# Kernel optimization log

Measured on AMD Instinct MI355X. Metric: run time of the kernel, lower is better.

The kernel has to match this reference:

```python
import jax, jax.numpy as jnp
import numpy as np

HOPS = 3  # C[i].weight tied to A[i+1].weight -> HOPS+1 distinct tables E_0..E_HOPS


def setup_inputs() -> dict:
    key = jax.random.key(0)
    ks = jax.random.split(key, 10)
    B, M, K, E, G, V = 32, 2048, 4, 128, 128, 50000
    s = 1.0 / np.sqrt(E).astype(np.float32)
    context = jax.random.randint(ks[0], (B, M, K), 0, V)          # memory (triples)
    h_ = jax.random.normal(ks[1], (B, G), dtype=jnp.float32)      # prev GRU hidden
    y_ = jax.random.randint(ks[2], (B,), 0, V)                    # prev token
    emb = jax.random.normal(ks[3], (HOPS + 1, V, E), dtype=jnp.float32) * 0.1
    W_ih = jax.random.normal(ks[4], (3 * G, E), dtype=jnp.float32) * s
    W_hh = jax.random.normal(ks[5], (3 * G, G), dtype=jnp.float32) * s
    b_ih = jax.random.normal(ks[6], (3 * G,), dtype=jnp.float32) * s
    b_hh = jax.random.normal(ks[7], (3 * G,), dtype=jnp.float32) * s
    W_vocab = jax.random.normal(ks[8], (V, 2 * E), dtype=jnp.float32) * s
    b_vocab = jax.random.normal(ks[9], (V,), dtype=jnp.float32) * s
    return dict(context=context, h_=h_, y_=y_, emb=emb, W_ih=W_ih, W_hh=W_hh,
                b_ih=b_ih, b_hh=b_hh, W_vocab=W_vocab, b_vocab=b_vocab)


def gru_cell(x, h, W_ih, W_hh, b_ih, b_hh):
    # PyTorch GRU cell semantics (r, z, n gate order).
    gi = x @ W_ih.T + b_ih
    gh = h @ W_hh.T + b_hh
    i_r, i_z, i_n = jnp.split(gi, 3, axis=-1)
    h_r, h_z, h_n = jnp.split(gh, 3, axis=-1)
    r = jax.nn.sigmoid(i_r + h_r)
    z = jax.nn.sigmoid(i_z + h_z)
    n = jnp.tanh(i_n + r * h_n)
    return (1.0 - z) * n + z * h


def reference(context, h_, y_, emb, W_ih, W_hh, b_ih, b_hh, W_vocab, b_vocab):
    x = emb[0][y_]                                   # [B, E] A[0] embed of prev token
    h = gru_cell(x, h_, W_ih, W_hh, b_ih, b_hh)      # [B, G], G == E
    q = h
    o1 = None
    attn = None
    for hop in range(HOPS):
        mA = emb[hop][context].sum(axis=2)           # gather [B,M,K,E] -> sum over K -> [B,M,E]
        p = jnp.einsum('bme,be->bm', mA, q)          # attention scores over memory slots
        attn = jax.nn.softmax(p, axis=1)             # [B, M]
        mC = emb[hop + 1][context].sum(axis=2)       # C[hop] table (tied to A[hop+1])
        o = jnp.einsum('bm,bme->be', attn, mC)       # memory read [B, E]
        q = q + o
        if hop == 0:
            o1 = o
    logits = jnp.concatenate([h, o1], axis=1) @ W_vocab.T + b_vocab  # [B, V]
    p_vocab = jax.nn.softmax(logits, axis=1)
    return h, p_vocab, attn
```

## Files before the change

kernel.cpp:

```cpp
#include <hip/hip_runtime.h>
#include <math.h>

#define BB 32
#define MM 2048
#define KK 4
#define EE 128
#define GG 128
#define VV 50000
#define HOPS 3

__global__ __launch_bounds__(384) void gru_kernel(
    const float* __restrict__ emb0,
    const int*   __restrict__ y,
    const float* __restrict__ hprev,
    const float* __restrict__ W_ih,
    const float* __restrict__ W_hh,
    const float* __restrict__ b_ih,
    const float* __restrict__ b_hh,
    float* __restrict__ h_out,
    float* __restrict__ q,
    float* __restrict__ o1)
{
    int b = blockIdx.x;
    int t = threadIdx.x;
    __shared__ float x[EE], h[GG], gi[3*GG], gh[3*GG];
    if (t < EE)            x[t]       = emb0[(size_t)y[b]*EE + t];
    else if (t < 2*EE)     h[t-EE]    = hprev[b*GG + (t-EE)];
    if (t < EE) o1[b*EE + t] = 0.f;
    __syncthreads();
    {
        float accI = b_ih[t], accH = b_hh[t];
        const float* wi = W_ih + (size_t)t*EE;
        const float* wh = W_hh + (size_t)t*GG;
        #pragma unroll 8
        for (int e = 0; e < EE; e++) { accI += x[e]*wi[e]; accH += h[e]*wh[e]; }
        gi[t] = accI; gh[t] = accH;
    }
    __syncthreads();
    if (t < GG) {
        float r = 1.f/(1.f + __expf(-(gi[t]        + gh[t])));
        float z = 1.f/(1.f + __expf(-(gi[GG+t]     + gh[GG+t])));
        float n = tanhf(gi[2*GG+t] + r*gh[2*GG+t]);
        float hn = (1.f - z)*n + z*h[t];
        h_out[b*GG + t] = hn;
        q[b*GG + t]     = hn;
    }
}

__global__ __launch_bounds__(256) void scores_kernel(
    const float* __restrict__ embT,
    const int*   __restrict__ ctx,
    const float* __restrict__ q,
    float* __restrict__ p)
{
    int gid  = blockIdx.x * 4 + (threadIdx.x >> 6);
    int lane = threadIdx.x & 63;
    int b    = gid >> 11;
    const int4 c = *(const int4*)(ctx + (size_t)gid*KK);
    float2 qv = *(const float2*)(q + b*EE + lane*2);
    float2 v0 = *(const float2*)(embT + (size_t)c.x*EE + lane*2);
    float2 v1 = *(const float2*)(embT + (size_t)c.y*EE + lane*2);
    float2 v2 = *(const float2*)(embT + (size_t)c.z*EE + lane*2);
    float2 v3 = *(const float2*)(embT + (size_t)c.w*EE + lane*2);
    float sx = v0.x + v1.x + v2.x + v3.x;
    float sy = v0.y + v1.y + v2.y + v3.y;
    float acc = sx*qv.x + sy*qv.y;
    #pragma unroll
    for (int off = 32; off; off >>= 1) acc += __shfl_down(acc, off);
    if (lane == 0) p[gid] = acc;
}

__global__ __launch_bounds__(256) void scores_s_kernel(
    const float* __restrict__ S,
    const float* __restrict__ q,
    float* __restrict__ p)
{
    int gid  = blockIdx.x * 4 + (threadIdx.x >> 6);
    int lane = threadIdx.x & 63;
    int b    = gid >> 11;
    float2 sv = *(const float2*)(S + (size_t)gid*EE + lane*2);
    float2 qv = *(const float2*)(q + b*EE + lane*2);
    float acc = sv.x*qv.x + sv.y*qv.y;
    #pragma unroll
    for (int off = 32; off; off >>= 1) acc += __shfl_down(acc, off);
    if (lane == 0) p[gid] = acc;
}

template<int WRITE_S, int SAVE_O1>
__global__ __launch_bounds__(256) void oacc_fused_kernel(
    const float* __restrict__ embT,
    const int*   __restrict__ ctx,
    const float* __restrict__ p,
    float* __restrict__ S_out,
    float* __restrict__ q,
    float* __restrict__ o1)
{
    int blk = blockIdx.x;
    int b = blk >> 5, s = blk & 31;
    int t = threadIdx.x;
    int w = t >> 6, lane = t & 63;

    const float* row = p + (size_t)b*MM;
    float v[8];
    float mx = -INFINITY;
    #pragma unroll
    for (int i = 0; i < 8; i++) { v[i] = row[t + i*256]; mx = fmaxf(mx, v[i]); }
    __shared__ float red[6];
    #pragma unroll
    for (int off = 32; off; off >>= 1) mx = fmaxf(mx, __shfl_down(mx, off));
    if (lane == 0) red[w] = mx;
    __syncthreads();
    if (t == 0) red[4] = fmaxf(fmaxf(red[0],red[1]), fmaxf(red[2],red[3]));
    __syncthreads();
    mx = red[4];
    float sum = 0.f;
    #pragma unroll
    for (int i = 0; i < 8; i++) sum += __expf(v[i] - mx);
    #pragma unroll
    for (int off = 32; off; off >>= 1) sum += __shfl_down(sum, off);
    __syncthreads();
    if (lane == 0) red[w] = sum;
    __syncthreads();
    if (t == 0) red[5] = 1.f / (red[0]+red[1]+red[2]+red[3]);
    __syncthreads();
    float rs = red[5];

    int m0 = s*64 + w*16;
    float ax = 0.f, ay = 0.f;
    for (int i = 0; i < 16; i++) {
        int m = m0 + i;
        float a = __expf(row[m] - mx) * rs;
        const int4 c = *(const int4*)(ctx + (size_t)(b*MM + m)*KK);
        float2 v0 = *(const float2*)(embT + (size_t)c.x*EE + lane*2);
        float2 v1 = *(const float2*)(embT + (size_t)c.y*EE + lane*2);
        float2 v2 = *(const float2*)(embT + (size_t)c.z*EE + lane*2);
        float2 v3 = *(const float2*)(embT + (size_t)c.w*EE + lane*2);
        float sx = v0.x + v1.x + v2.x + v3.x;
        float sy = v0.y + v1.y + v2.y + v3.y;
        if (WRITE_S)
            *(float2*)(S_out + ((size_t)b*MM + m)*EE + lane*2) = make_float2(sx, sy);
        ax += a * sx;
        ay += a * sy;
    }
    __shared__ float acc_red[4][EE];
    acc_red[w][lane*2]   = ax;
    acc_red[w][lane*2+1] = ay;
    __syncthreads();
    if (t < EE) {
        float vv = acc_red[0][t] + acc_red[1][t] + acc_red[2][t] + acc_red[3][t];
        atomicAdd(&q[b*EE + t], vv);
        if (SAVE_O1) atomicAdd(&o1[b*EE + t], vv);
    }
}

__global__ __launch_bounds__(256) void softmax_m_kernel(
    const float* __restrict__ p,
    float* __restrict__ attn)
{
    int b = blockIdx.x, t = threadIdx.x;
    const float* row = p + (size_t)b*MM;
    float v[8];
    float mx = -INFINITY;
    #pragma unroll
    for (int i = 0; i < 8; i++) { v[i] = row[t + i*256]; mx = fmaxf(mx, v[i]); }
    __shared__ float red[6];
    int w = t >> 6, lane = t & 63;
    #pragma unroll
    for (int off = 32; off; off >>= 1) mx = fmaxf(mx, __shfl_down(mx, off));
    if (lane == 0) red[w] = mx;
    __syncthreads();
    if (t == 0) { float m2 = fmaxf(fmaxf(red[0],red[1]), fmaxf(red[2],red[3])); red[4] = m2; }
    __syncthreads();
    mx = red[4];
    float sum = 0.f;
    #pragma unroll
    for (int i = 0; i < 8; i++) { v[i] = __expf(v[i] - mx); sum += v[i]; }
    #pragma unroll
    for (int off = 32; off; off >>= 1) sum += __shfl_down(sum, off);
    if (lane == 0) red[w] = sum;
    __syncthreads();
    if (t == 0) { red[5] = 1.f / (red[0]+red[1]+red[2]+red[3]); }
    __syncthreads();
    float rs = red[5];
    #pragma unroll
    for (int i = 0; i < 8; i++) attn[(size_t)b*MM + t + i*256] = v[i]*rs;
}

__global__ __launch_bounds__(256) void logits_kernel(
    const float* __restrict__ h,
    const float* __restrict__ o1,
    const float* __restrict__ Wv,
    const float* __restrict__ bv,
    float* __restrict__ logits)
{
    __shared__ float Ut[256][32];
    __shared__ float Wt[32][132];
    int t = threadIdx.x;
    for (int i = t; i < 256*32; i += 256) {
        int e = i >> 5, b = i & 31;
        Ut[e][b] = (e < GG) ? h[b*GG + e] : o1[b*EE + (e - GG)];
    }
    int vg = t & 31;
    int bg = t >> 5;
    int v0 = blockIdx.x * 128;
    float acc[4][4];
    #pragma unroll
    for (int i = 0; i < 4; i++)
        #pragma unroll
        for (int j = 0; j < 4; j++) acc[i][j] = 0.f;

    int vrow = t >> 1;
    int half = t & 1;
    const float* wrow = Wv + (size_t)(v0 + vrow)*256 + half*16;
    bool vok = (v0 + vrow) < VV;

    for (int ec = 0; ec < 256; ec += 32) {
        __syncthreads();
        #pragma unroll
        for (int j = 0; j < 4; j++) {
            float4 w = make_float4(0.f, 0.f, 0.f, 0.f);
            if (vok) w = *(const float4*)(wrow + ec + j*4);
            int e0 = half*16 + j*4;
            Wt[e0+0][vrow] = w.x;
            Wt[e0+1][vrow] = w.y;
            Wt[e0+2][vrow] = w.z;
            Wt[e0+3][vrow] = w.w;
        }
        __syncthreads();
        #pragma unroll 8
        for (int e = 0; e < 32; e++) {
            float4 w = *(const float4*)(&Wt[e][vg*4]);
            float4 u = *(const float4*)(&Ut[ec + e][bg*4]);
            acc[0][0] += w.x*u.x; acc[0][1] += w.x*u.y; acc[0][2] += w.x*u.z; acc[0][3] += w.x*u.w;
            acc[1][0] += w.y*u.x; acc[1][1] += w.y*u.y; acc[1][2] += w.y*u.z; acc[1][3] += w.y*u.w;
            acc[2][0] += w.z*u.x; acc[2][1] += w.z*u.y; acc[2][2] += w.z*u.z; acc[2][3] += w.z*u.w;
            acc[3][0] += w.w*u.x; acc[3][1] += w.w*u.y; acc[3][2] += w.w*u.z; acc[3][3] += w.w*u.w;
        }
    }
    #pragma unroll
    for (int i = 0; i < 4; i++) {
        int v = v0 + vg*4 + i;
        if (v < VV) {
            float bb = bv[v];
            #pragma unroll
            for (int j = 0; j < 4; j++)
                logits[(size_t)(bg*4 + j)*VV + v] = acc[i][j] + bb;
        }
    }
}

#define VCHUNK 6250
__global__ __launch_bounds__(256) void vpart_kernel(
    const float* __restrict__ logits,
    float* __restrict__ part)
{
    int blk = blockIdx.x;
    int b = blk >> 3, c = blk & 7;
    int t = threadIdx.x;
    const float* row = logits + (size_t)b*VV;
    int start = c*VCHUNK;
    int end   = min(start + VCHUNK, VV);
    __shared__ float red[4];
    int w = t >> 6, lane = t & 63;
    float mx = -INFINITY;
    for (int i = start + t; i < end; i += 256) mx = fmaxf(mx, row[i]);
    #pragma unroll
    for (int off = 32; off; off >>= 1) mx = fmaxf(mx, __shfl_down(mx, off));
    if (lane == 0) red[w] = mx;
    __syncthreads();
    float m = fmaxf(fmaxf(red[0], red[1]), fmaxf(red[2], red[3]));
    float sum = 0.f;
    for (int i = start + t; i < end; i += 256) sum += __expf(row[i] - m);
    #pragma unroll
    for (int off = 32; off; off >>= 1) sum += __shfl_down(sum, off);
    __syncthreads();
    if (lane == 0) red[w] = sum;
    __syncthreads();
    if (t == 0) {
        part[blk*2]   = m;
        part[blk*2+1] = red[0] + red[1] + red[2] + red[3];
    }
}

__global__ __launch_bounds__(256) void vfinal_kernel(
    float* __restrict__ logits,
    const float* __restrict__ part)
{
    int i = blockIdx.x*256 + threadIdx.x;
    if (i >= BB*VV) return;
    int b = i / VV;
    const float* pp = part + b*16;
    float M = -INFINITY;
    #pragma unroll
    for (int c = 0; c < 8; c++) M = fmaxf(M, pp[c*2]);
    float S = 0.f;
    #pragma unroll
    for (int c = 0; c < 8; c++) S += pp[c*2+1] * __expf(pp[c*2] - M);
    logits[i] = __expf(logits[i] - M) * (1.f / S);
}

extern "C" void kernel_launch(void* const* d_in, const int* in_sizes, int n_in,
                              void* d_out, int out_size, void* d_ws, size_t ws_size,
                              hipStream_t stream) {
    const int*   ctx    = (const int*)  d_in[0];
    const float* h_prev = (const float*)d_in[1];
    const int*   y      = (const int*)  d_in[2];
    const float* emb    = (const float*)d_in[3];
    const float* W_ih   = (const float*)d_in[4];
    const float* W_hh   = (const float*)d_in[5];
    const float* b_ih   = (const float*)d_in[6];
    const float* b_hh   = (const float*)d_in[7];
    const float* Wv     = (const float*)d_in[8];
    const float* bv     = (const float*)d_in[9];

    float* out_h    = (float*)d_out;
    float* out_pv   = out_h + BB*GG;
    float* out_attn = out_pv + (size_t)BB*VV;

    float* ws   = (float*)d_ws;
    float* q    = ws;
    float* o1   = q + BB*EE;
    float* p    = o1 + BB*EE;
    float* S    = p + BB*MM;
    float* part = S + (size_t)BB*MM*EE;

    gru_kernel<<<BB, 384, 0, stream>>>(emb, y, h_prev, W_ih, W_hh, b_ih, b_hh, out_h, q, o1);

    scores_kernel<<<(BB*MM)/4, 256, 0, stream>>>(emb, ctx, q, p);
    oacc_fused_kernel<1,1><<<BB*32, 256, 0, stream>>>(
        emb + (size_t)1*VV*EE, ctx, p, S, q, o1);

    scores_s_kernel<<<(BB*MM)/4, 256, 0, stream>>>(S, q, p);
    oacc_fused_kernel<1,0><<<BB*32, 256, 0, stream>>>(
        emb + (size_t)2*VV*EE, ctx, p, S, q, nullptr);

    scores_s_kernel<<<(BB*MM)/4, 256, 0, stream>>>(S, q, p);
    softmax_m_kernel<<<BB, 256, 0, stream>>>(p, out_attn);

    logits_kernel<<<(VV + 127)/128, 256, 0, stream>>>(out_h, o1, Wv, bv, out_pv);
    vpart_kernel<<<BB*8, 256, 0, stream>>>(out_pv, part);
    vfinal_kernel<<<(BB*VV + 255)/256, 256, 0, stream>>>(out_pv, part);
}
```

Measured before the change: 319.0 us.

## Gather all three embedding tables in one pass and stream precomputed sums

A single kernel now gathers context rows from tables 0, 1 and 2 at once, computes the first-hop scores, and writes the summed slot vectors for tables 1 and 2 into two workspace buffers. The attention-read kernels then stream those precomputed sums instead of re-gathering random embedding rows. This moves the scattered gathers into one wide, latency-overlapped pass and leaves the later hops with purely sequential reads. In exchange it writes an extra 32 MB workspace buffer, which adds write traffic and doubles the workspace footprint.

```diff
diff --git a/kernel.cpp b/kernel.cpp
--- a/kernel.cpp
+++ b/kernel.cpp
@@ -47,27 +47,51 @@
     }
 }
 
-__global__ __launch_bounds__(256) void scores_kernel(
-    const float* __restrict__ embT,
+__global__ __launch_bounds__(256) void gather_all_kernel(
+    const float* __restrict__ emb,
     const int*   __restrict__ ctx,
     const float* __restrict__ q,
-    float* __restrict__ p)
+    float* __restrict__ S1,
+    float* __restrict__ S2,
+    float* __restrict__ p0)
 {
     int gid  = blockIdx.x * 4 + (threadIdx.x >> 6);
     int lane = threadIdx.x & 63;
     int b    = gid >> 11;
     const int4 c = *(const int4*)(ctx + (size_t)gid*KK);
-    float2 qv = *(const float2*)(q + b*EE + lane*2);
-    float2 v0 = *(const float2*)(embT + (size_t)c.x*EE + lane*2);
-    float2 v1 = *(const float2*)(embT + (size_t)c.y*EE + lane*2);
-    float2 v2 = *(const float2*)(embT + (size_t)c.z*EE + lane*2);
-    float2 v3 = *(const float2*)(embT + (size_t)c.w*EE + lane*2);
-    float sx = v0.x + v1.x + v2.x + v3.x;
-    float sy = v0.y + v1.y + v2.y + v3.y;
-    float acc = sx*qv.x + sy*qv.y;
-    #pragma unroll
-    for (int off = 32; off; off >>= 1) acc += __shfl_down(acc, off);
-    if (lane == 0) p[gid] = acc;
+    int off = lane*2;
+    const float* e0 = emb;
+    const float* e1 = emb + (size_t)VV*EE;
+    const float* e2 = emb + (size_t)2*VV*EE;
+
+    float2 a0 = *(const float2*)(e0 + (size_t)c.x*EE + off);
+    float2 a1 = *(const float2*)(e0 + (size_t)c.y*EE + off);
+    float2 a2 = *(const float2*)(e0 + (size_t)c.z*EE + off);
+    float2 a3 = *(const float2*)(e0 + (size_t)c.w*EE + off);
+    float2 b0 = *(const float2*)(e1 + (size_t)c.x*EE + off);
+    float2 b1 = *(const float2*)(e1 + (size_t)c.y*EE + off);
+    float2 b2 = *(const float2*)(e1 + (size_t)c.z*EE + off);
+    float2 b3 = *(const float2*)(e1 + (size_t)c.w*EE + off);
+    float2 d0 = *(const float2*)(e2 + (size_t)c.x*EE + off);
+    float2 d1 = *(const float2*)(e2 + (size_t)c.y*EE + off);
+    float2 d2 = *(const float2*)(e2 + (size_t)c.z*EE + off);
+    float2 d3 = *(const float2*)(e2 + (size_t)c.w*EE + off);
+
+    float s0x = a0.x + a1.x + a2.x + a3.x;
+    float s0y = a0.y + a1.y + a2.y + a3.y;
+    float s1x = b0.x + b1.x + b2.x + b3.x;
+    float s1y = b0.y + b1.y + b2.y + b3.y;
+    float s2x = d0.x + d1.x + d2.x + d3.x;
+    float s2y = d0.y + d1.y + d2.y + d3.y;
+
+    *(float2*)(S1 + (size_t)gid*EE + off) = make_float2(s1x, s1y);
+    *(float2*)(S2 + (size_t)gid*EE + off) = make_float2(s2x, s2y);
+
+    float2 qv = *(const float2*)(q + b*EE + off);
+    float acc = s0x*qv.x + s0y*qv.y;
+    #pragma unroll
+    for (int o = 32; o; o >>= 1) acc += __shfl_down(acc, o);
+    if (lane == 0) p0[gid] = acc;
 }
 
 __global__ __launch_bounds__(256) void scores_s_kernel(
@@ -86,12 +110,10 @@
     if (lane == 0) p[gid] = acc;
 }
 
-template<int WRITE_S, int SAVE_O1>
-__global__ __launch_bounds__(256) void oacc_fused_kernel(
-    const float* __restrict__ embT,
-    const int*   __restrict__ ctx,
+template<int SAVE_O1>
+__global__ __launch_bounds__(256) void oacc_stream_kernel(
+    const float* __restrict__ S,
     const float* __restrict__ p,
-    float* __restrict__ S_out,
     float* __restrict__ q,
     float* __restrict__ o1)
 {
@@ -127,20 +149,13 @@
 
     int m0 = s*64 + w*16;
     float ax = 0.f, ay = 0.f;
+    #pragma unroll 4
     for (int i = 0; i < 16; i++) {
         int m = m0 + i;
         float a = __expf(row[m] - mx) * rs;
-        const int4 c = *(const int4*)(ctx + (size_t)(b*MM + m)*KK);
-        float2 v0 = *(const float2*)(embT + (size_t)c.x*EE + lane*2);
-        float2 v1 = *(const float2*)(embT + (size_t)c.y*EE + lane*2);
-        float2 v2 = *(const float2*)(embT + (size_t)c.z*EE + lane*2);
-        float2 v3 = *(const float2*)(embT + (size_t)c.w*EE + lane*2);
-        float sx = v0.x + v1.x + v2.x + v3.x;
-        float sy = v0.y + v1.y + v2.y + v3.y;
-        if (WRITE_S)
-            *(float2*)(S_out + ((size_t)b*MM + m)*EE + lane*2) = make_float2(sx, sy);
-        ax += a * sx;
-        ay += a * sy;
+        float2 sv = *(const float2*)(S + ((size_t)b*MM + m)*EE + lane*2);
+        ax += a * sv.x;
+        ay += a * sv.y;
     }
     __shared__ float acc_red[4][EE];
     acc_red[w][lane*2]   = ax;
@@ -321,20 +336,20 @@
     float* q    = ws;
     float* o1   = q + BB*EE;
     float* p    = o1 + BB*EE;
-    float* S    = p + BB*MM;
-    float* part = S + (size_t)BB*MM*EE;
+    float* S1   = p + BB*MM;
+    float* S2   = S1 + (size_t)BB*MM*EE;
+    float* part = S2 + (size_t)BB*MM*EE;
 
     gru_kernel<<<BB, 384, 0, stream>>>(emb, y, h_prev, W_ih, W_hh, b_ih, b_hh, out_h, q, o1);
 
-    scores_kernel<<<(BB*MM)/4, 256, 0, stream>>>(emb, ctx, q, p);
-    oacc_fused_kernel<1,1><<<BB*32, 256, 0, stream>>>(
-        emb + (size_t)1*VV*EE, ctx, p, S, q, o1);
-
-    scores_s_kernel<<<(BB*MM)/4, 256, 0, stream>>>(S, q, p);
-    oacc_fused_kernel<1,0><<<BB*32, 256, 0, stream>>>(
-        emb + (size_t)2*VV*EE, ctx, p, S, q, nullptr);
-
-    scores_s_kernel<<<(BB*MM)/4, 256, 0, stream>>>(S, q, p);
+    gather_all_kernel<<<(BB*MM)/4, 256, 0, stream>>>(emb, ctx, q, S1, S2, p);
+
+    oacc_stream_kernel<1><<<BB*32, 256, 0, stream>>>(S1, p, q, o1);
+
+    scores_s_kernel<<<(BB*MM)/4, 256, 0, stream>>>(S1, q, p);
+    oacc_stream_kernel<0><<<BB*32, 256, 0, stream>>>(S2, p, q, nullptr);
+
+    scores_s_kernel<<<(BB*MM)/4, 256, 0, stream>>>(S2, q, p);
     softmax_m_kernel<<<BB, 256, 0, stream>>>(p, out_attn);
 
     logits_kernel<<<(VV + 127)/128, 256, 0, stream>>>(out_h, o1, Wv, bv, out_pv);
```

Measured after the change: 323.4 us. No clear change (+1.4%).
